# Kernel optimization log

Measured on AMD Instinct MI355X. Metric: run time of the kernel, lower is better.

## Reference

```python
import jax, jax.numpy as jnp
import numpy as np

B, T, IN, H, OUT = 256, 100, 128, 1024, 35
BITS = 4
SLOPE = 25.0
THR_H = 1.0
THR_O = 1.0
BETA1, BETA2, BETA3, BETA4 = 0.9, 0.85, 0.8, 0.95


def fake_quant(w, w_min, w_max, bits=BITS):
    # FakeQuantize in training mode: STE -> forward value is quantized, grad passes through clamp
    levels = 2 ** bits
    scale = (w_max - w_min) / (levels - 1)
    wc = jnp.clip(w, w_min, w_max)
    q = jnp.round((wc - w_min) / scale) * scale + w_min
    return wc + jax.lax.stop_gradient(q - wc)


@jax.custom_vjp
def spike(x):
    # Heaviside forward, fast-sigmoid surrogate backward (snn.surrogate.fast_sigmoid)
    return (x > 0).astype(x.dtype)

def _spike_fwd(x):
    return (x > 0).astype(x.dtype), x

def _spike_bwd(x, g):
    return (g / (SLOPE * jnp.abs(x) + 1.0) ** 2,)

spike.defvjp(_spike_fwd, _spike_bwd)


def lif_step(cur, mem, beta, thr, reset_mechanism):
    # snntorch Leaky (reset_delay semantics): reset computed from previous mem, detached
    reset = jax.lax.stop_gradient((mem > thr).astype(cur.dtype))
    base = beta * mem + cur
    if reset_mechanism == "subtract":
        mem_new = base - reset * thr
    else:  # "zero"
        mem_new = base - reset * base
    spk = spike(mem_new - thr)
    return spk, mem_new


def setup_inputs() -> dict:
    key = jax.random.key(0)
    ks = jax.random.split(key, 5)
    x = jax.random.normal(ks[0], (B, T, IN), dtype=jnp.float32)
    # QuantLinear init: uniform(w_min, w_max); fc1 uses (-0.5, 0.5), others (0.001, 1.0)
    w1 = jax.random.uniform(ks[1], (H, IN), minval=-0.5, maxval=0.5, dtype=jnp.float32)
    w2 = jax.random.uniform(ks[2], (H, H), minval=0.001, maxval=1.0, dtype=jnp.float32)
    w3 = jax.random.uniform(ks[3], (H, H), minval=0.001, maxval=1.0, dtype=jnp.float32)
    w4 = jax.random.uniform(ks[4], (OUT, H), minval=0.001, maxval=1.0, dtype=jnp.float32)
    return {"x": x, "w1": w1, "w2": w2, "w3": w3, "w4": w4}


def reference(x, w1, w2, w3, w4):
    # hoist weight quantization out of the time loop (identical math each step)
    q1 = fake_quant(w1, -0.5, 0.5)
    q2 = fake_quant(w2, 0.001, 1.0)
    q3 = fake_quant(w3, 0.001, 1.0)
    q4 = fake_quant(w4, 0.001, 1.0)
    xs = jnp.transpose(x, (1, 0, 2)) / 15.0  # [T, B, IN]
    Bx = x.shape[0]

    def step(carry, xt):
        m1, m2, m3, m4 = carry
        s1, m1 = lif_step(xt @ q1.T, m1, BETA1, THR_H, "subtract")
        s2, m2 = lif_step(s1 @ q2.T, m2, BETA2, THR_H, "subtract")
        s3, m3 = lif_step(s2 @ q3.T, m3, BETA3, THR_H, "subtract")
        s4, m4 = lif_step(s3 @ q4.T, m4, BETA4, THR_O, "zero")
        return (m1, m2, m3, m4), (s1, s2, s3, s4, m4)

    init = (jnp.zeros((Bx, H), x.dtype), jnp.zeros((Bx, H), x.dtype),
            jnp.zeros((Bx, H), x.dtype), jnp.zeros((Bx, OUT), x.dtype))
    _, (spk1, spk2, spk3, spk4, mem4) = jax.lax.scan(step, init, xs)
    # stacked along time dim 0, matching torch.stack(dim=0)
    return spk1, spk2, spk3, spk4, mem4
```

## Files before the change

### kernel.cpp

```cpp
#include <hip/hip_runtime.h>
#include <stdint.h>

#define NB  256
#define NT  100
#define NIN 128
#define NH  1024
#define NOUT 35
#define MT  112

#define O_SPK2 26214400ull
#define O_SPK3 52428800ull
#define O_SPK4 78643200ull
#define O_MEM4 79539200ull

#define WS_SPK0 0ull
#define WS_SPK1 29360128ull
#define WS_K2B  58720256ull
#define WS_K3B  59768832ull
#define WS_K4B  60817408ull
#define WS_Q1T  60866560ull
#define WS_N1   61390848ull
#define WS_N2   61493248ull
#define WS_N3   61595648ull

#define S2C ((float)((1.0 - 0.001) / 15.0))
#define S1C ((float)(1.0 / 15.0))

typedef int v4i __attribute__((ext_vector_type(4)));

__device__ __forceinline__ void async16(const void* g, void* l) {
  __builtin_amdgcn_global_load_lds((const __attribute__((address_space(1))) uint32_t*)g,
                                   (__attribute__((address_space(3))) uint32_t*)l, 16, 0, 0);
}

__device__ __forceinline__ uint8_t qk(float w) {
  float wc = fminf(fmaxf(w, 0.001f), 1.0f);
  return (uint8_t)(int)rintf((wc - 0.001f) / S2C);
}

__global__ void k_prep(const float* __restrict__ w1, const float* __restrict__ w2,
                       const float* __restrict__ w3, const float* __restrict__ w4,
                       uint8_t* __restrict__ ws)
{
  long long id = (long long)blockIdx.x * 256 + threadIdx.x;
  if (id < 1048576) { ws[WS_K2B + id] = qk(w2[id]); return; }
  id -= 1048576;
  if (id < 1048576) { ws[WS_K3B + id] = qk(w3[id]); return; }
  id -= 1048576;
  if (id < 49152) {
    int j = (int)(id >> 10), i = (int)(id & 1023);
    ws[WS_K4B + id] = (j < NOUT) ? qk(w4[(size_t)j * 1024 + i]) : (uint8_t)0;
    return;
  }
  id -= 49152;
  if (id < 131072) {
    int i = (int)(id >> 10), j = (int)(id & 1023);
    float wv = w1[(size_t)j * 128 + i];
    float wc = fminf(fmaxf(wv, -0.5f), 0.5f);
    float q = rintf((wc + 0.5f) / S1C) * S1C - 0.5f;
    ((float*)(ws + WS_Q1T))[id] = q;
    return;
  }
  id -= 131072;
  if (id < 76800) ((uint32_t*)(ws + WS_N1))[id] = 0;
}

__global__ __launch_bounds__(256) void k_l1(const float* __restrict__ x,
                                            uint8_t* __restrict__ ws,
                                            float* __restrict__ out)
{
  __shared__ float lds[128 * 116 + 128 * 128];
  float* xsT = lds;
  float* qs  = lds + 128 * 116;
  float* cbuf = lds;
  const float* q1T = (const float*)(ws + WS_Q1T);
  uint8_t* spk0 = ws + WS_SPK0;
  uint32_t* n1 = (uint32_t*)(ws + WS_N1);

  const int b = blockIdx.x, jb = blockIdx.y;
  const int tid = threadIdx.x;
  const int ty = tid >> 4, tx = tid & 15;

  #pragma unroll
  for (int it = 0; it < 50; ++it) {
    int e = tid + it * 256;
    int t = e >> 7, i = e & 127;
    xsT[i * 116 + t] = x[(size_t)b * 12800 + e] / 15.0f;
  }
  #pragma unroll
  for (int it = 0; it < 32; ++it) {
    int e4 = (tid + it * 256) * 4;
    int i = e4 >> 7, j = e4 & 127;
    *(float4*)&qs[i * 128 + j] = *(const float4*)&q1T[(size_t)i * 1024 + jb * 128 + j];
  }
  __syncthreads();

  float acc[7][8];
  #pragma unroll
  for (int i = 0; i < 7; ++i)
    #pragma unroll
    for (int j = 0; j < 8; ++j) acc[i][j] = 0.f;

  #pragma unroll 4
  for (int k = 0; k < 128; ++k) {
    float a[7], q[8];
    #pragma unroll
    for (int i = 0; i < 7; ++i) a[i] = xsT[k * 116 + ty + 16 * i];
    #pragma unroll
    for (int j = 0; j < 8; ++j) q[j] = qs[k * 128 + tx + 16 * j];
    #pragma unroll
    for (int i = 0; i < 7; ++i)
      #pragma unroll
      for (int j = 0; j < 8; ++j)
        acc[i][j] = fmaf(a[i], q[j], acc[i][j]);
  }
  __syncthreads();
  #pragma unroll
  for (int i = 0; i < 7; ++i)
    #pragma unroll
    for (int j = 0; j < 8; ++j)
      cbuf[(ty + 16 * i) * 132 + tx + 16 * j] = acc[i][j];
  __syncthreads();

  if (tid < 128) {
    int j = tid;
    float m = 0.f;
    for (int t = 0; t < NT; ++t) {
      float c = cbuf[t * 132 + j];
      float rst = m > 1.0f ? 1.0f : 0.0f;
      m = fmaf(0.9f, m, c) - rst;
      bool sp = (m - 1.0f) > 0.0f;
      out[((size_t)t * NB + b) * NH + jb * 128 + j] = sp ? 1.0f : 0.0f;
      spk0[((size_t)b * MT + t) * 1024 + jb * 128 + j] = sp ? 1 : 0;
      unsigned long long bal = __ballot(sp);
      if ((tid & 63) == 0) atomicAdd((unsigned int*)&n1[t * NB + b], (unsigned)__popcll(bal));
    }
    for (int t = NT; t < MT; ++t)
      spk0[((size_t)b * MT + t) * 1024 + jb * 128 + j] = 0;
  }
}

__global__ __launch_bounds__(256) void k_l23(const uint8_t* __restrict__ Aspk,
                                             const uint8_t* __restrict__ Bq,
                                             const uint32_t* __restrict__ nprev,
                                             uint32_t* __restrict__ nout,
                                             float beta,
                                             float* __restrict__ outF,
                                             uint8_t* __restrict__ spkOut)
{
  __shared__ uint8_t lds[61440];
  __shared__ uint32_t nbuf[112];
  uint8_t* sA = lds;
  uint8_t* sB = lds + 28672;
  uint16_t* cbuf = (uint16_t*)lds;

  const int b = blockIdx.x, jb = blockIdx.y;
  const int tid = threadIdx.x, lane = tid & 63, wave = tid >> 6;
  const int lm = lane & 15, lk = lane >> 4;

  if (tid < NT) nbuf[tid] = nprev[tid * NB + b];

  const uint8_t* Ab = Aspk + (size_t)b * MT * 1024;
  const uint8_t* Bb = Bq + (size_t)jb * 128 * 1024;

  v4i acc[7][2];
  #pragma unroll
  for (int m = 0; m < 7; ++m)
    #pragma unroll
    for (int n = 0; n < 2; ++n) { acc[m][n][0]=0; acc[m][n][1]=0; acc[m][n][2]=0; acc[m][n][3]=0; }

  for (int kk = 0; kk < 1024; kk += 256) {
    __syncthreads();
    #pragma unroll
    for (int q = 0; q < 15; ++q) {
      int cid = wave * 15 + q;
      if (cid < 28) {
        int mt = cid >> 2, ks = cid & 3;
        async16(Ab + (size_t)(mt * 16 + lm) * 1024 + kk + ks * 64 + lk * 16, sA + cid * 1024);
      } else if (cid < 60) {
        int c2 = cid - 28, nt = c2 >> 2, ks = c2 & 3;
        async16(Bb + (size_t)(nt * 16 + lm) * 1024 + kk + ks * 64 + lk * 16, sB + c2 * 1024);
      }
    }
    __syncthreads();
    #pragma unroll
    for (int ks = 0; ks < 4; ++ks) {
      v4i bv0 = *(const v4i*)(sB + (size_t)((2 * wave) * 4 + ks) * 1024 + lane * 16);
      v4i bv1 = *(const v4i*)(sB + (size_t)((2 * wave + 1) * 4 + ks) * 1024 + lane * 16);
      #pragma unroll
      for (int m = 0; m < 7; ++m) {
        v4i av = *(const v4i*)(sA + (size_t)(m * 4 + ks) * 1024 + lane * 16);
        acc[m][0] = __builtin_amdgcn_mfma_i32_16x16x64_i8(av, bv0, acc[m][0], 0, 0, 0);
        acc[m][1] = __builtin_amdgcn_mfma_i32_16x16x64_i8(av, bv1, acc[m][1], 0, 0, 0);
      }
    }
  }
  __syncthreads();
  #pragma unroll
  for (int m = 0; m < 7; ++m)
    #pragma unroll
    for (int n = 0; n < 2; ++n)
      #pragma unroll
      for (int r = 0; r < 4; ++r) {
        int row = m * 16 + lk * 4 + r;
        int col = (2 * wave + n) * 16 + lm;
        cbuf[row * 132 + col] = (uint16_t)acc[m][n][r];
      }
  __syncthreads();

  if (tid < 128) {
    int j = tid;
    float m = 0.f;
    for (int t = 0; t < NT; ++t) {
      int kv = cbuf[t * 132 + j];
      float cur = fmaf(S2C, (float)kv, 0.001f * (float)nbuf[t]);
      float rst = m > 1.0f ? 1.0f : 0.0f;
      m = fmaf(beta, m, cur) - rst;
      bool sp = (m - 1.0f) > 0.0f;
      outF[((size_t)t * NB + b) * NH + jb * 128 + j] = sp ? 1.0f : 0.0f;
      spkOut[((size_t)b * MT + t) * 1024 + jb * 128 + j] = sp ? 1 : 0;
      unsigned long long bal = __ballot(sp);
      if ((tid & 63) == 0) atomicAdd((unsigned int*)&nout[t * NB + b], (unsigned)__popcll(bal));
    }
    for (int t = NT; t < MT; ++t)
      spkOut[((size_t)b * MT + t) * 1024 + jb * 128 + j] = 0;
  }
}

__global__ __launch_bounds__(256) void k_l4(const uint8_t* __restrict__ Aspk,
                                            const uint8_t* __restrict__ ws,
                                            float* __restrict__ out)
{
  __shared__ uint8_t lds[40960];
  __shared__ uint32_t nbuf[112];
  uint8_t* sA = lds;
  uint8_t* sB = lds + 28672;
  uint16_t* cbuf = (uint16_t*)lds;

  const int b = blockIdx.x;
  const int tid = threadIdx.x, lane = tid & 63, wave = tid >> 6;
  const int lm = lane & 15, lk = lane >> 4;
  const uint8_t* Bq = ws + WS_K4B;
  const uint32_t* n3 = (const uint32_t*)(ws + WS_N3);

  if (tid < NT) nbuf[tid] = n3[tid * NB + b];

  const uint8_t* Ab = Aspk + (size_t)b * MT * 1024;

  v4i acc[7];
  #pragma unroll
  for (int m = 0; m < 7; ++m) { acc[m][0]=0; acc[m][1]=0; acc[m][2]=0; acc[m][3]=0; }

  for (int kk = 0; kk < 1024; kk += 256) {
    __syncthreads();
    #pragma unroll
    for (int q = 0; q < 10; ++q) {
      int cid = wave * 10 + q;
      if (cid < 28) {
        int mt = cid >> 2, ks = cid & 3;
        async16(Ab + (size_t)(mt * 16 + lm) * 1024 + kk + ks * 64 + lk * 16, sA + cid * 1024);
      } else if (cid < 40) {
        int c2 = cid - 28, nt = c2 >> 2, ks = c2 & 3;
        async16(Bq + (size_t)(nt * 16 + lm) * 1024 + kk + ks * 64 + lk * 16, sB + c2 * 1024);
      }
    }
    __syncthreads();
    if (wave < 3) {
      #pragma unroll
      for (int ks = 0; ks < 4; ++ks) {
        v4i bv = *(const v4i*)(sB + (size_t)(wave * 4 + ks) * 1024 + lane * 16);
        #pragma unroll
        for (int m = 0; m < 7; ++m) {
          v4i av = *(const v4i*)(sA + (size_t)(m * 4 + ks) * 1024 + lane * 16);
          acc[m] = __builtin_amdgcn_mfma_i32_16x16x64_i8(av, bv, acc[m], 0, 0, 0);
        }
      }
    }
  }
  __syncthreads();
  if (wave < 3) {
    #pragma unroll
    for (int m = 0; m < 7; ++m)
      #pragma unroll
      for (int r = 0; r < 4; ++r) {
        int row = m * 16 + lk * 4 + r;
        int col = wave * 16 + lm;
        cbuf[row * 52 + col] = (uint16_t)acc[m][r];
      }
  }
  __syncthreads();

  if (tid < NOUT) {
    int j = tid;
    float m = 0.f;
    for (int t = 0; t < NT; ++t) {
      int kv = cbuf[t * 52 + j];
      float cur = fmaf(S2C, (float)kv, 0.001f * (float)nbuf[t]);
      float rst = m > 1.0f ? 1.0f : 0.0f;
      float bsv = fmaf(0.95f, m, cur);
      m = (rst > 0.0f) ? 0.0f : bsv;
      size_t rowO = ((size_t)t * NB + b) * NOUT + j;
      out[O_SPK4 + rowO] = ((m - 1.0f) > 0.0f) ? 1.0f : 0.0f;
      out[O_MEM4 + rowO] = m;
    }
  }
}

extern "C" void kernel_launch(void* const* d_in, const int* in_sizes, int n_in,
                              void* d_out, int out_size, void* d_ws, size_t ws_size,
                              hipStream_t stream)
{
  const float* x  = (const float*)d_in[0];
  const float* w1 = (const float*)d_in[1];
  const float* w2 = (const float*)d_in[2];
  const float* w3 = (const float*)d_in[3];
  const float* w4 = (const float*)d_in[4];
  float* out = (float*)d_out;
  uint8_t* ws = (uint8_t*)d_ws;

  uint8_t* SPK0 = ws + WS_SPK0;
  uint8_t* SPK1 = ws + WS_SPK1;
  uint32_t* N1 = (uint32_t*)(ws + WS_N1);
  uint32_t* N2 = (uint32_t*)(ws + WS_N2);
  uint32_t* N3 = (uint32_t*)(ws + WS_N3);

  hipLaunchKernelGGL(k_prep, dim3(9196), dim3(256), 0, stream, w1, w2, w3, w4, ws);
  hipLaunchKernelGGL(k_l1,  dim3(256, 8), dim3(256), 0, stream, x, ws, out);
  hipLaunchKernelGGL(k_l23, dim3(256, 8), dim3(256), 0, stream,
                     SPK0, ws + WS_K2B, N1, N2, 0.85f, out + O_SPK2, SPK1);
  hipLaunchKernelGGL(k_l23, dim3(256, 8), dim3(256), 0, stream,
                     SPK1, ws + WS_K3B, N2, N3, 0.8f, out + O_SPK3, SPK0);
  hipLaunchKernelGGL(k_l4,  dim3(256), dim3(256), 0, stream, SPK0, ws, out);
}
```

Baseline: 838.2 us.

## Split layer-1 into separate current GEMM and membrane scan kernels

Replaces the fused layer-1 kernel, which ran a 128-column GEMM per batch and then a serial time scan on only half the threads, with two kernels. The first computes the input currents for every (t, b) row into the spk1 output buffer. The second runs the LIF scan with all 256 threads per block over 256 neurons, prefetching the next current. This uses more threads for the scan, at the cost of an extra launch and a round trip of the fp32 current tensor through global memory.

New measurement: 727.5 us. 1.15x faster.

```diff
diff --git a/kernel.cpp b/kernel.cpp
--- a/kernel.cpp
+++ b/kernel.cpp
@@ -65,79 +65,90 @@
   if (id < 76800) ((uint32_t*)(ws + WS_N1))[id] = 0;
 }
 
-__global__ __launch_bounds__(256) void k_l1(const float* __restrict__ x,
-                                            uint8_t* __restrict__ ws,
-                                            float* __restrict__ out)
-{
-  __shared__ float lds[128 * 116 + 128 * 128];
-  float* xsT = lds;
-  float* qs  = lds + 128 * 116;
-  float* cbuf = lds;
+__global__ __launch_bounds__(256) void k_cur1(const float* __restrict__ x,
+                                              const uint8_t* __restrict__ ws,
+                                              float* __restrict__ out)
+{
+  __shared__ float xsT[128 * 68];
+  __shared__ float qch[16 * 256];
   const float* q1T = (const float*)(ws + WS_Q1T);
+  const int tid = threadIdx.x;
+  const int rb = blockIdx.x >> 2, cb = blockIdx.x & 3;
+  const int t = rb >> 2, b0 = (rb & 3) * 64;
+  const int jI = tid & 63, rI = tid >> 6;
+  const int j4 = jI * 4, r16 = rI * 16;
+
+  #pragma unroll
+  for (int k = 0; k < 32; ++k) {
+    int e = tid + k * 256;
+    int r = e >> 7, i = e & 127;
+    xsT[i * 68 + r] = x[((size_t)(b0 + r) * NT + t) * NIN + i] / 15.0f;
+  }
+  float acc[16][4];
+  #pragma unroll
+  for (int d = 0; d < 16; ++d) { acc[d][0]=0.f; acc[d][1]=0.f; acc[d][2]=0.f; acc[d][3]=0.f; }
+  for (int ic = 0; ic < 8; ++ic) {
+    __syncthreads();
+    #pragma unroll
+    for (int k = 0; k < 16; ++k) {
+      int e = tid + k * 256;
+      int ii = e >> 8, j = e & 255;
+      qch[ii * 256 + j] = q1T[((size_t)(ic * 16 + ii) << 10) + cb * 256 + j];
+    }
+    __syncthreads();
+    #pragma unroll
+    for (int ii = 0; ii < 16; ++ii) {
+      int i = ic * 16 + ii;
+      const float4 q  = *(const float4*)&qch[ii * 256 + j4];
+      const float4 xa = *(const float4*)&xsT[i * 68 + r16];
+      const float4 xb = *(const float4*)&xsT[i * 68 + r16 + 4];
+      const float4 xc = *(const float4*)&xsT[i * 68 + r16 + 8];
+      const float4 xd = *(const float4*)&xsT[i * 68 + r16 + 12];
+      float xr[16];
+      xr[0]=xa.x; xr[1]=xa.y; xr[2]=xa.z; xr[3]=xa.w;
+      xr[4]=xb.x; xr[5]=xb.y; xr[6]=xb.z; xr[7]=xb.w;
+      xr[8]=xc.x; xr[9]=xc.y; xr[10]=xc.z; xr[11]=xc.w;
+      xr[12]=xd.x; xr[13]=xd.y; xr[14]=xd.z; xr[15]=xd.w;
+      #pragma unroll
+      for (int d = 0; d < 16; ++d) {
+        acc[d][0] = fmaf(xr[d], q.x, acc[d][0]);
+        acc[d][1] = fmaf(xr[d], q.y, acc[d][1]);
+        acc[d][2] = fmaf(xr[d], q.z, acc[d][2]);
+        acc[d][3] = fmaf(xr[d], q.w, acc[d][3]);
+      }
+    }
+  }
+  #pragma unroll
+  for (int d = 0; d < 16; ++d) {
+    float4 v = make_float4(acc[d][0], acc[d][1], acc[d][2], acc[d][3]);
+    *(float4*)&out[((size_t)rb * 64 + r16 + d) * 1024 + cb * 256 + j4] = v;
+  }
+}
+
+__global__ __launch_bounds__(256) void k_scan1(uint8_t* __restrict__ ws, float* __restrict__ out)
+{
+  const int tid = threadIdx.x;
+  const int b = blockIdx.x >> 2;
+  const int j = (blockIdx.x & 3) * 256 + tid;
   uint8_t* spk0 = ws + WS_SPK0;
   uint32_t* n1 = (uint32_t*)(ws + WS_N1);
-
-  const int b = blockIdx.x, jb = blockIdx.y;
-  const int tid = threadIdx.x;
-  const int ty = tid >> 4, tx = tid & 15;
-
-  #pragma unroll
-  for (int it = 0; it < 50; ++it) {
-    int e = tid + it * 256;
-    int t = e >> 7, i = e & 127;
-    xsT[i * 116 + t] = x[(size_t)b * 12800 + e] / 15.0f;
-  }
-  #pragma unroll
-  for (int it = 0; it < 32; ++it) {
-    int e4 = (tid + it * 256) * 4;
-    int i = e4 >> 7, j = e4 & 127;
-    *(float4*)&qs[i * 128 + j] = *(const float4*)&q1T[(size_t)i * 1024 + jb * 128 + j];
-  }
-  __syncthreads();
-
-  float acc[7][8];
-  #pragma unroll
-  for (int i = 0; i < 7; ++i)
-    #pragma unroll
-    for (int j = 0; j < 8; ++j) acc[i][j] = 0.f;
-
-  #pragma unroll 4
-  for (int k = 0; k < 128; ++k) {
-    float a[7], q[8];
-    #pragma unroll
-    for (int i = 0; i < 7; ++i) a[i] = xsT[k * 116 + ty + 16 * i];
-    #pragma unroll
-    for (int j = 0; j < 8; ++j) q[j] = qs[k * 128 + tx + 16 * j];
-    #pragma unroll
-    for (int i = 0; i < 7; ++i)
-      #pragma unroll
-      for (int j = 0; j < 8; ++j)
-        acc[i][j] = fmaf(a[i], q[j], acc[i][j]);
-  }
-  __syncthreads();
-  #pragma unroll
-  for (int i = 0; i < 7; ++i)
-    #pragma unroll
-    for (int j = 0; j < 8; ++j)
-      cbuf[(ty + 16 * i) * 132 + tx + 16 * j] = acc[i][j];
-  __syncthreads();
-
-  if (tid < 128) {
-    int j = tid;
-    float m = 0.f;
-    for (int t = 0; t < NT; ++t) {
-      float c = cbuf[t * 132 + j];
-      float rst = m > 1.0f ? 1.0f : 0.0f;
-      m = fmaf(0.9f, m, c) - rst;
-      bool sp = (m - 1.0f) > 0.0f;
-      out[((size_t)t * NB + b) * NH + jb * 128 + j] = sp ? 1.0f : 0.0f;
-      spk0[((size_t)b * MT + t) * 1024 + jb * 128 + j] = sp ? 1 : 0;
-      unsigned long long bal = __ballot(sp);
-      if ((tid & 63) == 0) atomicAdd((unsigned int*)&n1[t * NB + b], (unsigned)__popcll(bal));
-    }
-    for (int t = NT; t < MT; ++t)
-      spk0[((size_t)b * MT + t) * 1024 + jb * 128 + j] = 0;
-  }
+  const size_t stride = (size_t)NB * NH;
+  size_t idx = (size_t)b * NH + j;
+  size_t sidx = (size_t)b * MT * 1024 + j;
+  float m = 0.f;
+  float c = out[idx];
+  for (int t = 0; t < NT; ++t) {
+    float cn = (t + 1 < NT) ? out[idx + stride] : 0.f;
+    float rst = m > 1.0f ? 1.0f : 0.0f;
+    m = fmaf(0.9f, m, c) - rst;
+    bool sp = (m - 1.0f) > 0.0f;
+    out[idx] = sp ? 1.0f : 0.0f;
+    spk0[sidx] = sp ? 1 : 0;
+    unsigned long long bal = __ballot(sp);
+    if ((tid & 63) == 0) atomicAdd((unsigned int*)&n1[t * NB + b], (unsigned)__popcll(bal));
+    idx += stride; sidx += 1024; c = cn;
+  }
+  for (int t = NT; t < MT; ++t) { spk0[sidx] = 0; sidx += 1024; }
 }
 
 __global__ __launch_bounds__(256) void k_l23(const uint8_t* __restrict__ Aspk,
@@ -325,7 +336,8 @@
   uint32_t* N3 = (uint32_t*)(ws + WS_N3);
 
   hipLaunchKernelGGL(k_prep, dim3(9196), dim3(256), 0, stream, w1, w2, w3, w4, ws);
-  hipLaunchKernelGGL(k_l1,  dim3(256, 8), dim3(256), 0, stream, x, ws, out);
+  hipLaunchKernelGGL(k_cur1, dim3(1600), dim3(256), 0, stream, x, ws, out);
+  hipLaunchKernelGGL(k_scan1, dim3(1024), dim3(256), 0, stream, ws, out);
   hipLaunchKernelGGL(k_l23, dim3(256, 8), dim3(256), 0, stream,
                      SPK0, ws + WS_K2B, N1, N2, 0.85f, out + O_SPK2, SPK1);
   hipLaunchKernelGGL(k_l23, dim3(256, 8), dim3(256), 0, stream,
```
